# Kernel tuning notes

Hardware: AMD Instinct MI355X
Metric: run time of the kernel (lower is better)

Reference implementation:

```python
import jax, jax.numpy as jnp
import numpy as np

BN_EPS = 1e-5


def setup_inputs() -> dict:
    key = jax.random.key(0)
    ks = jax.random.split(key, 8)
    B, C, H, W = 2, 512, 64, 64
    Ck, Cv = 256, 256
    x = jax.random.normal(ks[0], (B, C, H, W), jnp.float32)
    # f_key/f_query shared 1x1 conv (kaiming, relu)
    wk = jax.random.normal(ks[1], (Ck, C), jnp.float32) * (2.0 / C) ** 0.5
    bk = jnp.zeros((Ck,), jnp.float32)
    bn_gamma = jax.random.uniform(ks[2], (Ck,), jnp.float32, 0.5, 1.5)
    bn_beta = jax.random.normal(ks[3], (Ck,), jnp.float32) * 0.1
    bn_mean = jax.random.normal(ks[4], (Ck,), jnp.float32) * 0.1
    bn_var = jax.random.uniform(ks[5], (Ck,), jnp.float32, 0.5, 1.5)
    # f_value: 3x3 conv then 1x1 conv
    wv1 = jax.random.normal(ks[6], (Cv, C, 3, 3), jnp.float32) * (2.0 / (C * 9)) ** 0.5
    bv1 = jnp.zeros((Cv,), jnp.float32)
    wv2 = jax.random.normal(ks[7], (Cv, Cv), jnp.float32) * (2.0 / Cv) ** 0.5
    bv2 = jnp.zeros((Cv,), jnp.float32)
    return dict(x=x, wk=wk, bk=bk, bn_gamma=bn_gamma, bn_beta=bn_beta,
                bn_mean=bn_mean, bn_var=bn_var, wv1=wv1, bv1=bv1, wv2=wv2, bv2=bv2)


def reference(x, wk, bk, bn_gamma, bn_beta, bn_mean, bn_var, wv1, bv1, wv2, bv2):
    B, C, H, W = x.shape
    Ck, Cv = wk.shape[0], wv1.shape[0]
    N = H * W
    # f_key == f_query: 1x1 conv + BN (inference form) + ReLU
    feat = jnp.einsum('oc,bchw->bohw', wk, x) + bk[:, None, None]
    scale_bn = (bn_gamma / jnp.sqrt(bn_var + BN_EPS))
    feat = (feat - bn_mean[:, None, None]) * scale_bn[:, None, None] + bn_beta[:, None, None]
    feat = jax.nn.relu(feat).reshape(B, Ck, N)  # [B, Ck, N]
    # sim_map = softmax(Ck^-0.5 * Q^T K); Q and K are the same tensor
    sim_map = jax.nn.softmax(jnp.einsum('bcn,bcm->bnm', feat, feat) * (Ck ** -0.5), axis=-1)
    # f_value: conv3x3 + relu + conv1x1 + relu
    v = jax.lax.conv_general_dilated(x, wv1, (1, 1), 'SAME',
                                     dimension_numbers=('NCHW', 'OIHW', 'NCHW'))
    v = jax.nn.relu(v + bv1[:, None, None])
    v = jax.nn.relu(jnp.einsum('oc,bchw->bohw', wv2, v) + bv2[:, None, None])
    v = v.reshape(B, Cv, N)  # [B, Cv, N]
    context = jnp.einsum('bnm,bcm->bcn', sim_map, v).reshape(B, Cv, H, W)
    return context, sim_map
```

## Files before the change

### kernel.cpp

```cpp
#include <hip/hip_runtime.h>
#include <hip/hip_bf16.h>
#include <stdint.h>

typedef unsigned short u16_t;
typedef __attribute__((ext_vector_type(8))) short short8;
typedef __attribute__((ext_vector_type(4))) float f32x4;
typedef __attribute__((ext_vector_type(4))) unsigned short us4;

__device__ __forceinline__ float bf2f(u16_t u) {
  union { unsigned int i; float f; } c; c.i = ((unsigned int)u) << 16; return c.f;
}
__device__ __forceinline__ u16_t f2bf(float f) {
  union { float f; unsigned int i; } c; c.f = f;
  unsigned int x = c.i;
  unsigned int r = x + 0x7fffu + ((x >> 16) & 1u);
  return (u16_t)(r >> 16);
}

__device__ __forceinline__ void gload_lds16(const u16_t* g, u16_t* l) {
  __builtin_amdgcn_global_load_lds(
      (const __attribute__((address_space(1))) void*)g,
      (__attribute__((address_space(3))) void*)(unsigned int)(uintptr_t)l,
      16, 0, 0);
}

struct Seg {
  const u16_t* Ah;
  const u16_t* Al;
  const u16_t* Bh;
  const u16_t* Bl;
  int boff;
};

struct GemmArgs {
  Seg segs[9];
  int nseg;
  int segs_per_split;
  int K;
  int ldA, ldB;
  long long sA, sB;
  float alpha;
  float* outf;
  long long sOut;
  long long sSplit;
  int ldT;
};

template<int BM, int BN, int MODE, bool PADB, bool SYMM, int NCH = 4>
__global__ __launch_bounds__(256, 4) void gemm_tn(GemmArgs args) {
  constexpr int FM = BM / 32, FN = BN / 32;
  constexpr int AH_E = NCH * BM * 8;
  constexpr int AL_E = (MODE == 0) ? NCH * BM * 8 : 8;
  constexpr int BH_E = NCH * BN * 8;
  constexpr int BL_E = (MODE <= 1) ? NCH * BN * 8 : 8;
  constexpr int SM_E = AH_E + AL_E + BH_E + BL_E;
  static_assert(!SYMM || (size_t)SM_E * 2 >= 32 * 132 * 4, "tbuf alias too small");
  __shared__ __align__(16) u16_t smem[SM_E];
  u16_t* aflat_h = smem;
  u16_t* aflat_l = smem + AH_E;
  u16_t* bflat_h = smem + AH_E + AL_E;
  u16_t* bflat_l = smem + AH_E + AL_E + BH_E;

  const int tid = threadIdx.x;
  const int wave = tid >> 6, lane = tid & 63;
  const int lhi = lane >> 4, llo = lane & 15;
  const int wr = wave >> 1, wc = wave & 1;
  int nt, mt, b, split;
  if (SYMM) {
    b = blockIdx.z; split = 0;
    int t = blockIdx.x, r = 0;
    while (t >= 32 - r) { t -= 32 - r; ++r; }
    mt = r; nt = r + t;
  } else {
    nt = blockIdx.x; mt = blockIdx.y;
    b = blockIdx.z & 1; split = blockIdx.z >> 1;
  }
  const int row0 = mt * BM, col0 = nt * BN;

  f32x4 acc[FM][FN];
  const f32x4 zero4 = {0.f, 0.f, 0.f, 0.f};
#pragma unroll
  for (int i = 0; i < FM; ++i)
#pragma unroll
    for (int j = 0; j < FN; ++j) acc[i][j] = zero4;

  constexpr int RA = BM * NCH / 256;
  constexpr int RB = BN * NCH / 256;

  const int s0 = split * args.segs_per_split;
  int s1 = s0 + args.segs_per_split;
  if (s1 > args.nseg) s1 = args.nseg;

  for (int s = s0; s < s1; ++s) {
    const u16_t* Abh = args.segs[s].Ah + (size_t)b * args.sA;
    const u16_t* Abl = args.segs[s].Al + (size_t)b * args.sA;
    const u16_t* Bbh = args.segs[s].Bh + (size_t)b * args.sB;
    const u16_t* Bbl = args.segs[s].Bl + (size_t)b * args.sB;
    const int boff = args.segs[s].boff;
    for (int k0 = 0; k0 < args.K; k0 += NCH * 8) {
      __syncthreads();
#pragma unroll
      for (int r = 0; r < RA; ++r) {
        int idx = r * 256 + tid;
        int chunk = idx / BM, m = idx % BM;
        size_t goff = (size_t)(row0 + m) * args.ldA + (k0 + chunk * 8);
        gload_lds16(Abh + goff, aflat_h + (size_t)idx * 8);
        if (MODE == 0)
          gload_lds16(Abl + goff, aflat_l + (size_t)idx * 8);
      }
#pragma unroll
      for (int r = 0; r < RB; ++r) {
        int idx = r * 256 + tid;
        int chunk = idx / BN, n = idx % BN;
        long long rowi;
        if (PADB) {
          int gn = col0 + n;
          rowi = (long long)((gn >> 6) + 1) * 66 + (gn & 63) + 1 + boff;
        } else {
          rowi = col0 + n;
        }
        size_t goff = (size_t)rowi * args.ldB + (k0 + chunk * 8);
        gload_lds16(Bbh + goff, bflat_h + (size_t)idx * 8);
        if (MODE <= 1)
          gload_lds16(Bbl + goff, bflat_l + (size_t)idx * 8);
      }
      __syncthreads();
#pragma unroll
      for (int kk = 0; kk < NCH / 4; ++kk) {
        const int ckA = (kk * 4 + lhi) * BM;
        const int ckB = (kk * 4 + lhi) * BN;
        short8 afh[FM], afl[FM], bfh[FN], bfl[FN];
#pragma unroll
        for (int i = 0; i < FM; ++i) {
          afh[i] = *(const short8*)(aflat_h + ((size_t)ckA + wr * (BM / 2) + i * 16 + llo) * 8);
          if (MODE == 0)
            afl[i] = *(const short8*)(aflat_l + ((size_t)ckA + wr * (BM / 2) + i * 16 + llo) * 8);
        }
#pragma unroll
        for (int j = 0; j < FN; ++j) {
          bfh[j] = *(const short8*)(bflat_h + ((size_t)ckB + wc * (BN / 2) + j * 16 + llo) * 8);
          if (MODE <= 1)
            bfl[j] = *(const short8*)(bflat_l + ((size_t)ckB + wc * (BN / 2) + j * 16 + llo) * 8);
        }
#pragma unroll
        for (int i = 0; i < FM; ++i)
#pragma unroll
          for (int j = 0; j < FN; ++j) {
            f32x4 t = acc[i][j];
            if (MODE <= 1)
              t = __builtin_amdgcn_mfma_f32_16x16x32_bf16(afh[i], bfl[j], t, 0, 0, 0);
            if (MODE == 0)
              t = __builtin_amdgcn_mfma_f32_16x16x32_bf16(afl[i], bfh[j], t, 0, 0, 0);
            t = __builtin_amdgcn_mfma_f32_16x16x32_bf16(afh[i], bfh[j], t, 0, 0, 0);
            acc[i][j] = t;
          }
      }
    }
  }

  float* outp = args.outf + (size_t)split * args.sSplit + (size_t)b * args.sOut;
#pragma unroll
  for (int i = 0; i < FM; ++i) {
    int mb = row0 + wr * (BM / 2) + i * 16 + lhi * 4;
#pragma unroll
    for (int j = 0; j < FN; ++j) {
      int n = col0 + wc * (BN / 2) + j * 16 + llo;
      f32x4 vv = acc[i][j] * args.alpha;
      *(f32x4*)(outp + (size_t)n * args.ldT + mb) = vv;
    }
  }
  if (SYMM) {
    if (nt != mt) {
      float* tb = (float*)smem;
#pragma unroll
      for (int i = 0; i < FM; ++i) {
        __syncthreads();
#pragma unroll
        for (int j = 0; j < FN; ++j) {
#pragma unroll
          for (int r2 = 0; r2 < 4; ++r2) {
            int trow = wr * 16 + lhi * 4 + r2;
            int tcol = wc * 64 + j * 16 + llo;
            tb[trow * 132 + tcol] = acc[i][j][r2] * args.alpha;
          }
        }
        __syncthreads();
#pragma unroll
        for (int it = 0; it < 4; ++it) {
          int idx = it * 256 + tid;
          int row = idx >> 5, c4 = idx & 31;
          int mg = row0 + (row >> 4) * 64 + i * 16 + (row & 15);
          f32x4 v4 = *(f32x4*)&tb[row * 132 + c4 * 4];
          *(f32x4*)(outp + (size_t)mg * args.ldT + col0 + c4 * 4) = v4;
        }
      }
    }
  }
}

struct Conv3Args {
  const u16_t* W;
  const u16_t* X;
  float* outf;
  long long sOut;
  long long sSplit;
};
__global__ __launch_bounds__(256, 4) void conv3_gemm(Conv3Args a) {
  __shared__ __align__(16) u16_t lA[3][4][128][8];
  __shared__ __align__(16) u16_t lB[4 * 144 * 8];
  const int tid = threadIdx.x;
  const int wave = tid >> 6, lane = tid & 63;
  const int lhi = lane >> 4, llo = lane & 15;
  const int wr = wave >> 1, wc = wave & 1;
  const int nt = blockIdx.x, mt = blockIdx.y;
  const int b = blockIdx.z & 1, ty = blockIdx.z >> 1;
  const int row0 = mt * 128;
  const int base = (2 * nt + ty) * 66;
  const u16_t* Xb = a.X + (size_t)b * 4356 * 512;
  const u16_t* Wt = a.W + (size_t)(ty * 3) * 131072;

  f32x4 acc[4][4];
  const f32x4 zero4 = {0.f, 0.f, 0.f, 0.f};
#pragma unroll
  for (int i = 0; i < 4; ++i)
#pragma unroll
    for (int j = 0; j < 4; ++j) acc[i][j] = zero4;

  for (int k0 = 0; k0 < 512; k0 += 32) {
    __syncthreads();
#pragma unroll
    for (int t = 0; t < 3; ++t)
#pragma unroll
      for (int r = 0; r < 2; ++r) {
        int slot = r * 256 + tid;
        int chunk = slot >> 7, m = slot & 127;
        const u16_t* src = Wt + (size_t)t * 131072 + (size_t)(row0 + m) * 512 + k0 + chunk * 8;
        gload_lds16(src, &lA[t][0][0][0] + (size_t)slot * 8);
      }
#pragma unroll
    for (int r = 0; r < 2; ++r) {
      int idx = r * 256 + tid;
      int chunk = idx / 144, rr = idx % 144;
      gload_lds16(Xb + (size_t)(base + rr) * 512 + k0 + chunk * 8, lB + (size_t)idx * 8);
    }
    if (tid < 64) {
      int idx = 512 + tid;
      int chunk = idx / 144, rr = idx % 144;
      gload_lds16(Xb + (size_t)(base + rr) * 512 + k0 + chunk * 8, lB + (size_t)idx * 8);
    }
    __syncthreads();
#pragma unroll
    for (int t = 0; t < 3; ++t) {
      short8 af[4], bf[4];
#pragma unroll
      for (int i = 0; i < 4; ++i)
        af[i] = *(const short8*)&lA[t][lhi][wr * 64 + i * 16 + llo][0];
#pragma unroll
      for (int j = 0; j < 4; ++j) {
        int rB = wc * 66 + j * 16 + llo + t;
        bf[j] = *(const short8*)(lB + ((size_t)lhi * 144 + rB) * 8);
      }
#pragma unroll
      for (int i = 0; i < 4; ++i)
#pragma unroll
        for (int j = 0; j < 4; ++j)
          acc[i][j] = __builtin_amdgcn_mfma_f32_16x16x32_bf16(af[i], bf[j], acc[i][j], 0, 0, 0);
    }
  }

  float* outp = a.outf + (size_t)ty * a.sSplit + (size_t)b * a.sOut;
#pragma unroll
  for (int i = 0; i < 4; ++i) {
    int mb = row0 + wr * 64 + i * 16 + lhi * 4;
#pragma unroll
    for (int j = 0; j < 4; ++j) {
      int n = (nt << 7) + wc * 64 + j * 16 + llo;
      *(f32x4*)(outp + (size_t)n * 256 + mb) = acc[i][j];
    }
  }
}

template<int LDT, bool PER_COL>
__global__ __launch_bounds__(256) void reduce_split(
    const float* __restrict__ part, long long sSplit, int ns,
    const float* __restrict__ scale, const float* __restrict__ bias,
    u16_t* __restrict__ oh, u16_t* __restrict__ ol, long long total) {
  long long i = ((long long)blockIdx.x * 256 + threadIdx.x) * 4;
  if (i >= total) return;
  f32x4 s = *(const f32x4*)(part + i);
  for (int p = 1; p < ns; ++p) s += *(const f32x4*)(part + (size_t)p * sSplit + i);
  f32x4 v;
  if (PER_COL) {
    int c = (int)(i & (LDT - 1));
    f32x4 bi = *(const f32x4*)(bias + c);
    if (scale) { f32x4 sc = *(const f32x4*)(scale + c); v = s * sc + bi; }
    else v = s + bi;
  } else {
    int r = (int)((i / LDT) & 255);
    float bi = bias[r];
    v = s + bi;
  }
  us4 h, l;
#pragma unroll
  for (int c2 = 0; c2 < 4; ++c2) {
    float vv = v[c2] > 0.f ? v[c2] : 0.f;
    u16_t hh = f2bf(vv);
    h[c2] = hh;
    l[c2] = f2bf(vv - bf2f(hh));
  }
  *(us4*)(oh + i) = h;
  if (ol) *(us4*)(ol + i) = l;
}

__global__ __launch_bounds__(256) void reduce_split_f32(
    const float* __restrict__ part, long long sSplit, int ns,
    float* __restrict__ out, long long total) {
  long long i = ((long long)blockIdx.x * 256 + threadIdx.x) * 4;
  if (i >= total) return;
  f32x4 s = *(const f32x4*)(part + i);
  for (int p = 1; p < ns; ++p) s += *(const f32x4*)(part + (size_t)p * sSplit + i);
  *(f32x4*)(out + i) = s;
}

__global__ __launch_bounds__(256) void softmax_k(float* S, u16_t* P) {
  const int row = blockIdx.x;
  float* Sr = S + (size_t)row * 4096;
  u16_t* Pr = P + (size_t)row * 4096;
  const int t = threadIdx.x;
  const int wave = t >> 6;
  f32x4 v[4];
  float vmax = -3.4e38f;
#pragma unroll
  for (int i = 0; i < 4; ++i) {
    v[i] = ((const f32x4*)Sr)[t + i * 256];
#pragma unroll
    for (int c = 0; c < 4; ++c) vmax = fmaxf(vmax, v[i][c]);
  }
#pragma unroll
  for (int off = 32; off; off >>= 1) vmax = fmaxf(vmax, __shfl_xor(vmax, off));
  __shared__ float red[4];
  if ((t & 63) == 0) red[wave] = vmax;
  __syncthreads();
  vmax = fmaxf(fmaxf(red[0], red[1]), fmaxf(red[2], red[3]));
  float sum = 0.f;
#pragma unroll
  for (int i = 0; i < 4; ++i)
#pragma unroll
    for (int c = 0; c < 4; ++c) { v[i][c] = __expf(v[i][c] - vmax); sum += v[i][c]; }
#pragma unroll
  for (int off = 32; off; off >>= 1) sum += __shfl_xor(sum, off);
  __shared__ float red2[4];
  if ((t & 63) == 0) red2[wave] = sum;
  __syncthreads();
  sum = red2[0] + red2[1] + red2[2] + red2[3];
  float rs = 1.0f / sum;
#pragma unroll
  for (int i = 0; i < 4; ++i) {
    f32x4 o = v[i] * rs;
    ((f32x4*)Sr)[t + i * 256] = o;
    us4 pb;
#pragma unroll
    for (int c = 0; c < 4; ++c) pb[c] = f2bf(o[c]);
    ((us4*)Pr)[t + i * 256] = pb;
  }
}

__global__ __launch_bounds__(256) void xprep(const float* __restrict__ x,
                                             u16_t* __restrict__ xh, u16_t* __restrict__ xl) {
  __shared__ float tile[64][65];
  const int b = blockIdx.z, c0 = blockIdx.y * 64, n0 = blockIdx.x * 64;
  const float* xb = x + ((size_t)b * 512 + c0) * 4096 + n0;
  const int t = threadIdx.x;
  const int tr = t >> 6, tc = t & 63;
#pragma unroll
  for (int rr = 0; rr < 16; ++rr) {
    int ci = tr + rr * 4;
    tile[ci][tc] = xb[(size_t)ci * 4096 + tc];
  }
  __syncthreads();
#pragma unroll
  for (int rr = 0; rr < 16; ++rr) {
    int nj = rr * 4 + tr;
    float v = tile[tc][nj];
    size_t rp = (size_t)(blockIdx.x + 1) * 66 + nj + 1;
    size_t o = ((size_t)b * 4356 + rp) * 512 + c0 + tc;
    u16_t hh = f2bf(v);
    xh[o] = hh;
    xl[o] = f2bf(v - bf2f(hh));
  }
}

__global__ __launch_bounds__(256) void prep_all(
    const float* __restrict__ wk, const float* __restrict__ wv2, const float* __restrict__ wv1,
    const float* __restrict__ g, const float* __restrict__ be, const float* __restrict__ mu,
    const float* __restrict__ var, const float* __restrict__ bkb,
    u16_t* __restrict__ wkh, u16_t* __restrict__ wkl,
    u16_t* __restrict__ w2h, u16_t* __restrict__ w2l,
    u16_t* __restrict__ w1h, float* __restrict__ bnA, float* __restrict__ bnB,
    u16_t* __restrict__ xh, u16_t* __restrict__ xl) {
  long long i = (long long)blockIdx.x * 256 + threadIdx.x;
  if (i < 256) {
    float s = g[i] * rsqrtf(var[i] + 1e-5f);
    bnA[i] = s;
    bnB[i] = (bkb[i] - mu[i]) * s + be[i];
    return;
  }
  i -= 256;
  if (i < 131072) {
    float v = wk[i];
    u16_t hh = f2bf(v);
    wkh[i] = hh; wkl[i] = f2bf(v - bf2f(hh));
    return;
  }
  i -= 131072;
  if (i < 65536) {
    float v = wv2[i];
    u16_t hh = f2bf(v);
    w2h[i] = hh; w2l[i] = f2bf(v - bf2f(hh));
    return;
  }
  i -= 65536;
  if (i < 1179648) {
    int tp = (int)(i / (256 * 512));
    int rem = (int)(i % (256 * 512));
    int o = rem / 512, c = rem % 512;
    w1h[i] = f2bf(wv1[((size_t)o * 512 + c) * 9 + tp]);
    return;
  }
  i -= 1179648;
  if (i < 133120) {
    int blk = (int)(i >> 8), t = (int)(i & 255);
    int rowi = blk % 260, b = blk / 260;
    int rp;
    if (rowi < 66) rp = rowi;
    else if (rowi < 132) rp = 4290 + (rowi - 66);
    else { int g2 = (rowi - 132) >> 1; rp = (g2 + 1) * 66 + ((rowi - 132) & 1) * 65; }
    size_t base = ((size_t)b * 4356 + rp) * 512;
    const us4 z = {0, 0, 0, 0};
    if (t < 128) *(us4*)(xh + base + (size_t)t * 4) = z;
    else *(us4*)(xl + base + (size_t)(t - 128) * 4) = z;
  }
}

extern "C" void kernel_launch(void* const* d_in, const int* in_sizes, int n_in,
                              void* d_out, int out_size, void* d_ws, size_t ws_size,
                              hipStream_t stream) {
  (void)in_sizes; (void)n_in; (void)out_size; (void)ws_size;
  const float* x   = (const float*)d_in[0];
  const float* wk  = (const float*)d_in[1];
  const float* bk  = (const float*)d_in[2];
  const float* gam = (const float*)d_in[3];
  const float* bet = (const float*)d_in[4];
  const float* mu  = (const float*)d_in[5];
  const float* var = (const float*)d_in[6];
  const float* wv1 = (const float*)d_in[7];
  const float* bv1 = (const float*)d_in[8];
  const float* wv2 = (const float*)d_in[9];
  const float* bv2 = (const float*)d_in[10];

  const int B = 2;
  const size_t XT_E  = (size_t)B * 4356 * 512;
  const size_t WK_E  = 256 * 512;
  const size_t WV1_E = 9ull * 256 * 512;
  const size_t WV2_E = 256 * 256;
  const size_t FT_E  = (size_t)B * 4096 * 256;
  const size_t P_E   = (size_t)B * 4096 * 4096;

  size_t off = 0;
  auto carve = [&](size_t bytes) -> char* {
    off = (off + 255) & ~(size_t)255;
    char* p = (char*)d_ws + off;
    off += bytes;
    return p;
  };
  u16_t* xh  = (u16_t*)carve(XT_E * 2);
  u16_t* xl  = (u16_t*)carve(XT_E * 2);
  u16_t* wkh = (u16_t*)carve(WK_E * 2);
  u16_t* wkl = (u16_t*)carve(WK_E * 2);
  u16_t* w1h = (u16_t*)carve(WV1_E * 2);
  u16_t* w2h = (u16_t*)carve(WV2_E * 2);
  u16_t* w2l = (u16_t*)carve(WV2_E * 2);
  u16_t* fth = (u16_t*)carve(FT_E * 2);
  u16_t* ftl = (u16_t*)carve(FT_E * 2);
  u16_t* v1h = (u16_t*)carve(FT_E * 2);
  u16_t* v1l = (u16_t*)carve(FT_E * 2);
  u16_t* vh  = (u16_t*)carve(FT_E * 2);
  u16_t* Pb  = (u16_t*)carve(P_E * 2);
  float* bnA = (float*)carve(256 * 4);
  float* bnB = (float*)carve(256 * 4);

  float* big_part = (float*)Pb;
  float* pv_part  = (float*)d_ws;

  float* ctx = (float*)d_out;
  float* sim = (float*)d_out + (size_t)B * 256 * 4096;

  const long long FT_LL = (long long)FT_E;

  prep_all<<<5897, 256, 0, stream>>>(wk, wv2, wv1, gam, bet, mu, var, bk,
                                     wkh, wkl, w2h, w2l, w1h, bnA, bnB, xh, xl);
  xprep<<<dim3(64, 8, 2), 256, 0, stream>>>(x, xh, xl);

  {
    GemmArgs a = {};
    a.segs[0] = {wkh,       wkl,       xh,       xl,       0};
    a.segs[1] = {wkh + 256, wkl + 256, xh + 256, xl + 256, 0};
    a.nseg = 2; a.segs_per_split = 1; a.K = 256; a.ldA = 512; a.ldB = 512;
    a.sA = 0; a.sB = (long long)4356 * 512; a.alpha = 1.f;
    a.outf = big_part; a.sOut = (long long)4096 * 256; a.sSplit = FT_LL; a.ldT = 256;
    gemm_tn<64, 128, 0, true, false><<<dim3(32, 4, 4), 256, 0, stream>>>(a);
    reduce_split<256, true><<<2048, 256, 0, stream>>>(big_part, FT_LL, 2, bnA, bnB, fth, ftl, FT_LL);
  }
  {
    GemmArgs a = {};
    a.segs[0] = {fth, nullptr, fth, ftl, 0};
    a.nseg = 1; a.segs_per_split = 1; a.K = 256; a.ldA = 256; a.ldB = 256;
    a.sA = (long long)4096 * 256; a.sB = (long long)4096 * 256; a.alpha = 0.0625f;
    a.outf = sim; a.sOut = (long long)4096 * 4096; a.sSplit = 0; a.ldT = 4096;
    gemm_tn<128, 128, 1, false, true><<<dim3(528, 1, 2), 256, 0, stream>>>(a);
  }
  {
    Conv3Args a;
    a.W = w1h; a.X = xh;
    a.outf = big_part; a.sOut = (long long)4096 * 256; a.sSplit = FT_LL;
    conv3_gemm<<<dim3(32, 2, 6), 256, 0, stream>>>(a);
    reduce_split<256, true><<<2048, 256, 0, stream>>>(big_part, FT_LL, 3, nullptr, bv1, v1h, v1l, FT_LL);
  }
  {
    GemmArgs a = {};
    a.segs[0] = {v1h,       v1l,       w2h,       w2l,       0};
    a.segs[1] = {v1h + 128, v1l + 128, w2h + 128, w2l + 128, 0};
    a.nseg = 2; a.segs_per_split = 1; a.K = 128; a.ldA = 256; a.ldB = 256;
    a.sA = (long long)4096 * 256; a.sB = 0; a.alpha = 1.f;
    a.outf = big_part; a.sOut = (long long)256 * 4096; a.sSplit = FT_LL; a.ldT = 4096;
    gemm_tn<128, 64, 0, false, false><<<dim3(4, 32, 4), 256, 0, stream>>>(a);
    reduce_split<4096, false><<<2048, 256, 0, stream>>>(big_part, FT_LL, 2, nullptr, bv2, vh, nullptr, FT_LL);
  }
  softmax_k<<<B * 4096, 256, 0, stream>>>(sim, Pb);
  {
    GemmArgs a = {};
    for (int q = 0; q < 4; ++q)
      a.segs[q] = {Pb + (size_t)q * 1024, nullptr, vh + (size_t)q * 1024, nullptr, 0};
    a.nseg = 4; a.segs_per_split = 1; a.K = 1024; a.ldA = 4096; a.ldB = 4096;
    a.sA = (long long)4096 * 4096; a.sB = (long long)256 * 4096; a.alpha = 1.f;
    a.outf = pv_part; a.sOut = (long long)256 * 4096; a.sSplit = FT_LL; a.ldT = 4096;
    gemm_tn<128, 128, 2, false, false, 8><<<dim3(2, 32, 8), 256, 0, stream>>>(a);
    reduce_split_f32<<<2048, 256, 0, stream>>>(pv_part, FT_LL, 4, ctx, FT_LL);
  }
}
```

Before: 265.9 us.

## Fuse softmax into symmetric QK GEMM via recompute with partial row stats

After: 295.4 us. 11.1% more time.

```diff
diff --git a/kernel.cpp b/kernel.cpp
--- a/kernel.cpp
+++ b/kernel.cpp
@@ -46,7 +46,7 @@
   int ldT;
 };
 
-template<int BM, int BN, int MODE, bool PADB, bool SYMM, int NCH = 4>
+template<int BM, int BN, int MODE, bool PADB, int NCH = 4>
 __global__ __launch_bounds__(256, 4) void gemm_tn(GemmArgs args) {
   constexpr int FM = BM / 32, FN = BN / 32;
   constexpr int AH_E = NCH * BM * 8;
@@ -54,7 +54,6 @@
   constexpr int BH_E = NCH * BN * 8;
   constexpr int BL_E = (MODE <= 1) ? NCH * BN * 8 : 8;
   constexpr int SM_E = AH_E + AL_E + BH_E + BL_E;
-  static_assert(!SYMM || (size_t)SM_E * 2 >= 32 * 132 * 4, "tbuf alias too small");
   __shared__ __align__(16) u16_t smem[SM_E];
   u16_t* aflat_h = smem;
   u16_t* aflat_l = smem + AH_E;
@@ -65,16 +64,8 @@
   const int wave = tid >> 6, lane = tid & 63;
   const int lhi = lane >> 4, llo = lane & 15;
   const int wr = wave >> 1, wc = wave & 1;
-  int nt, mt, b, split;
-  if (SYMM) {
-    b = blockIdx.z; split = 0;
-    int t = blockIdx.x, r = 0;
-    while (t >= 32 - r) { t -= 32 - r; ++r; }
-    mt = r; nt = r + t;
-  } else {
-    nt = blockIdx.x; mt = blockIdx.y;
-    b = blockIdx.z & 1; split = blockIdx.z >> 1;
-  }
+  const int nt = blockIdx.x, mt = blockIdx.y;
+  const int b = blockIdx.z & 1, split = blockIdx.z >> 1;
   const int row0 = mt * BM, col0 = nt * BN;
 
   f32x4 acc[FM][FN];
@@ -169,19 +160,191 @@
       *(f32x4*)(outp + (size_t)n * args.ldT + mb) = vv;
     }
   }
-  if (SYMM) {
-    if (nt != mt) {
+}
+
+struct QkArgs {
+  const u16_t* fh;
+  const u16_t* fl;
+  float* pmax;
+  float* psum;
+  const float* mx;
+  const float* rs;
+  float* sim;
+  u16_t* Pb;
+};
+
+template<int EPI>
+__global__ __launch_bounds__(256, 4) void qk_symm(QkArgs args) {
+  __shared__ __align__(16) u16_t smem[3 * 4096];
+  u16_t* aflat_h = smem;
+  u16_t* bflat_h = smem + 4096;
+  u16_t* bflat_l = smem + 8192;
+
+  const int tid = threadIdx.x;
+  const int wave = tid >> 6, lane = tid & 63;
+  const int lhi = lane >> 4, llo = lane & 15;
+  const int wr = wave >> 1, wc = wave & 1;
+  const int b = blockIdx.z;
+  int t = blockIdx.x, r = 0;
+  while (t >= 32 - r) { t -= 32 - r; ++r; }
+  const int mt = r, nt = r + t;
+  const int row0 = mt * 128, col0 = nt * 128;
+
+  const u16_t* Fh = args.fh + (size_t)b * 4096 * 256;
+  const u16_t* Fl = args.fl + (size_t)b * 4096 * 256;
+
+  f32x4 acc[4][4];
+  const f32x4 zero4 = {0.f, 0.f, 0.f, 0.f};
+#pragma unroll
+  for (int i = 0; i < 4; ++i)
+#pragma unroll
+    for (int j = 0; j < 4; ++j) acc[i][j] = zero4;
+
+  for (int k0 = 0; k0 < 256; k0 += 32) {
+    __syncthreads();
+#pragma unroll
+    for (int rr = 0; rr < 2; ++rr) {
+      int idx = rr * 256 + tid;
+      int chunk = idx >> 7, m = idx & 127;
+      gload_lds16(Fh + (size_t)(row0 + m) * 256 + k0 + chunk * 8, aflat_h + (size_t)idx * 8);
+      gload_lds16(Fh + (size_t)(col0 + m) * 256 + k0 + chunk * 8, bflat_h + (size_t)idx * 8);
+      gload_lds16(Fl + (size_t)(col0 + m) * 256 + k0 + chunk * 8, bflat_l + (size_t)idx * 8);
+    }
+    __syncthreads();
+    short8 afh[4], bfh[4], bfl[4];
+#pragma unroll
+    for (int i = 0; i < 4; ++i)
+      afh[i] = *(const short8*)(aflat_h + ((size_t)lhi * 128 + wr * 64 + i * 16 + llo) * 8);
+#pragma unroll
+    for (int j = 0; j < 4; ++j) {
+      bfh[j] = *(const short8*)(bflat_h + ((size_t)lhi * 128 + wc * 64 + j * 16 + llo) * 8);
+      bfl[j] = *(const short8*)(bflat_l + ((size_t)lhi * 128 + wc * 64 + j * 16 + llo) * 8);
+    }
+#pragma unroll
+    for (int i = 0; i < 4; ++i)
+#pragma unroll
+      for (int j = 0; j < 4; ++j) {
+        f32x4 tt = acc[i][j];
+        tt = __builtin_amdgcn_mfma_f32_16x16x32_bf16(afh[i], bfl[j], tt, 0, 0, 0);
+        tt = __builtin_amdgcn_mfma_f32_16x16x32_bf16(afh[i], bfh[j], tt, 0, 0, 0);
+        acc[i][j] = tt;
+      }
+  }
+#pragma unroll
+  for (int i = 0; i < 4; ++i)
+#pragma unroll
+    for (int j = 0; j < 4; ++j) acc[i][j] *= 0.0625f;
+
+  if (EPI == 0) {
+    __syncthreads();
+    float* nmax_l = (float*)smem;
+    float* nsum_l = nmax_l + 256;
+    float* mmax_l = nsum_l + 256;
+    float* msum_l = mmax_l + 256;
+#pragma unroll
+    for (int j = 0; j < 4; ++j) {
+      float m_ = -3.4e38f;
+#pragma unroll
+      for (int i = 0; i < 4; ++i)
+#pragma unroll
+        for (int r2 = 0; r2 < 4; ++r2) m_ = fmaxf(m_, acc[i][j][r2]);
+      m_ = fmaxf(m_, __shfl_xor(m_, 16));
+      m_ = fmaxf(m_, __shfl_xor(m_, 32));
+      float su = 0.f;
+#pragma unroll
+      for (int i = 0; i < 4; ++i)
+#pragma unroll
+        for (int r2 = 0; r2 < 4; ++r2) su += __expf(acc[i][j][r2] - m_);
+      su += __shfl_xor(su, 16);
+      su += __shfl_xor(su, 32);
+      if (lhi == 0) {
+        int nl = wc * 64 + j * 16 + llo;
+        nmax_l[wr * 128 + nl] = m_;
+        nsum_l[wr * 128 + nl] = su;
+      }
+    }
+    if (mt != nt) {
+#pragma unroll
+      for (int i = 0; i < 4; ++i)
+#pragma unroll
+        for (int r2 = 0; r2 < 4; ++r2) {
+          float m_ = fmaxf(fmaxf(acc[0][0][r2], 0.f) * 0.f - 3.4e38f, -3.4e38f);
+          m_ = -3.4e38f;
+#pragma unroll
+          for (int j = 0; j < 4; ++j) m_ = fmaxf(m_, acc[i][j][r2]);
+          m_ = fmaxf(m_, __shfl_xor(m_, 1));
+          m_ = fmaxf(m_, __shfl_xor(m_, 2));
+          m_ = fmaxf(m_, __shfl_xor(m_, 4));
+          m_ = fmaxf(m_, __shfl_xor(m_, 8));
+          float su = 0.f;
+#pragma unroll
+          for (int j = 0; j < 4; ++j) su += __expf(acc[i][j][r2] - m_);
+          su += __shfl_xor(su, 1);
+          su += __shfl_xor(su, 2);
+          su += __shfl_xor(su, 4);
+          su += __shfl_xor(su, 8);
+          if (llo == 0) {
+            int ml = wr * 64 + i * 16 + lhi * 4 + r2;
+            mmax_l[wc * 128 + ml] = m_;
+            msum_l[wc * 128 + ml] = su;
+          }
+        }
+    }
+    __syncthreads();
+    if (tid < 128) {
+      float a0 = nmax_l[tid], a1 = nmax_l[128 + tid];
+      float g = fmaxf(a0, a1);
+      float su = nsum_l[tid] * __expf(a0 - g) + nsum_l[128 + tid] * __expf(a1 - g);
+      size_t o = (size_t)mt * 8192 + (size_t)b * 4096 + col0 + tid;
+      args.pmax[o] = g;
+      args.psum[o] = su;
+    } else if (mt != nt) {
+      int ml = tid - 128;
+      float a0 = mmax_l[ml], a1 = mmax_l[128 + ml];
+      float g = fmaxf(a0, a1);
+      float su = msum_l[ml] * __expf(a0 - g) + msum_l[128 + ml] * __expf(a1 - g);
+      size_t o = (size_t)nt * 8192 + (size_t)b * 4096 + row0 + ml;
+      args.pmax[o] = g;
+      args.psum[o] = su;
+    }
+  } else {
+    const float* MX = args.mx + (size_t)b * 4096;
+    const float* RS = args.rs + (size_t)b * 4096;
+    float* simb = args.sim + (size_t)b * 4096 * 4096;
+    u16_t* Pbb = args.Pb + (size_t)b * 4096 * 4096;
+#pragma unroll
+    for (int i = 0; i < 4; ++i) {
+      int mb = row0 + wr * 64 + i * 16 + lhi * 4;
+#pragma unroll
+      for (int j = 0; j < 4; ++j) {
+        int n = col0 + wc * 64 + j * 16 + llo;
+        float mxn = MX[n], rsn = RS[n];
+        f32x4 o;
+        us4 h;
+#pragma unroll
+        for (int r2 = 0; r2 < 4; ++r2) {
+          float e = __expf(acc[i][j][r2] - mxn) * rsn;
+          o[r2] = e;
+          h[r2] = f2bf(e);
+        }
+        *(f32x4*)(simb + (size_t)n * 4096 + mb) = o;
+        *(us4*)(Pbb + (size_t)n * 4096 + mb) = h;
+      }
+    }
+    if (mt != nt) {
       float* tb = (float*)smem;
 #pragma unroll
-      for (int i = 0; i < FM; ++i) {
+      for (int i = 0; i < 4; ++i) {
         __syncthreads();
 #pragma unroll
-        for (int j = 0; j < FN; ++j) {
-#pragma unroll
-          for (int r2 = 0; r2 < 4; ++r2) {
-            int trow = wr * 16 + lhi * 4 + r2;
+        for (int r2 = 0; r2 < 4; ++r2) {
+          int m = row0 + wr * 64 + i * 16 + lhi * 4 + r2;
+          float mxm = MX[m], rsm = RS[m];
+          int trow = wr * 16 + lhi * 4 + r2;
+#pragma unroll
+          for (int j = 0; j < 4; ++j) {
             int tcol = wc * 64 + j * 16 + llo;
-            tb[trow * 132 + tcol] = acc[i][j][r2] * args.alpha;
+            tb[trow * 132 + tcol] = __expf(acc[i][j][r2] - mxm) * rsm;
           }
         }
         __syncthreads();
@@ -191,11 +354,30 @@
           int row = idx >> 5, c4 = idx & 31;
           int mg = row0 + (row >> 4) * 64 + i * 16 + (row & 15);
           f32x4 v4 = *(f32x4*)&tb[row * 132 + c4 * 4];
-          *(f32x4*)(outp + (size_t)mg * args.ldT + col0 + c4 * 4) = v4;
+          *(f32x4*)(simb + (size_t)mg * 4096 + col0 + c4 * 4) = v4;
+          us4 h;
+#pragma unroll
+          for (int c = 0; c < 4; ++c) h[c] = f2bf(v4[c]);
+          *(us4*)(Pbb + (size_t)mg * 4096 + col0 + c4 * 4) = h;
         }
       }
     }
   }
+}
+
+__global__ __launch_bounds__(256) void stat_reduce(
+    const float* __restrict__ pmax, const float* __restrict__ psum,
+    float* __restrict__ mx, float* __restrict__ rs) {
+  int row = blockIdx.x * 256 + threadIdx.x;
+  float g = -3.4e38f;
+#pragma unroll
+  for (int c = 0; c < 32; ++c) g = fmaxf(g, pmax[(size_t)c * 8192 + row]);
+  float su = 0.f;
+#pragma unroll
+  for (int c = 0; c < 32; ++c)
+    su += psum[(size_t)c * 8192 + row] * __expf(pmax[(size_t)c * 8192 + row] - g);
+  mx[row] = g;
+  rs[row] = 1.0f / su;
 }
 
 struct Conv3Args {
@@ -322,49 +504,6 @@
   *(f32x4*)(out + i) = s;
 }
 
-__global__ __launch_bounds__(256) void softmax_k(float* S, u16_t* P) {
-  const int row = blockIdx.x;
-  float* Sr = S + (size_t)row * 4096;
-  u16_t* Pr = P + (size_t)row * 4096;
-  const int t = threadIdx.x;
-  const int wave = t >> 6;
-  f32x4 v[4];
-  float vmax = -3.4e38f;
-#pragma unroll
-  for (int i = 0; i < 4; ++i) {
-    v[i] = ((const f32x4*)Sr)[t + i * 256];
-#pragma unroll
-    for (int c = 0; c < 4; ++c) vmax = fmaxf(vmax, v[i][c]);
-  }
-#pragma unroll
-  for (int off = 32; off; off >>= 1) vmax = fmaxf(vmax, __shfl_xor(vmax, off));
-  __shared__ float red[4];
-  if ((t & 63) == 0) red[wave] = vmax;
-  __syncthreads();
-  vmax = fmaxf(fmaxf(red[0], red[1]), fmaxf(red[2], red[3]));
-  float sum = 0.f;
-#pragma unroll
-  for (int i = 0; i < 4; ++i)
-#pragma unroll
-    for (int c = 0; c < 4; ++c) { v[i][c] = __expf(v[i][c] - vmax); sum += v[i][c]; }
-#pragma unroll
-  for (int off = 32; off; off >>= 1) sum += __shfl_xor(sum, off);
-  __shared__ float red2[4];
-  if ((t & 63) == 0) red2[wave] = sum;
-  __syncthreads();
-  sum = red2[0] + red2[1] + red2[2] + red2[3];
-  float rs = 1.0f / sum;
-#pragma unroll
-  for (int i = 0; i < 4; ++i) {
-    f32x4 o = v[i] * rs;
-    ((f32x4*)Sr)[t + i * 256] = o;
-    us4 pb;
-#pragma unroll
-    for (int c = 0; c < 4; ++c) pb[c] = f2bf(o[c]);
-    ((us4*)Pr)[t + i * 256] = pb;
-  }
-}
-
 __global__ __launch_bounds__(256) void xprep(const float* __restrict__ x,
                                              u16_t* __restrict__ xh, u16_t* __restrict__ xl) {
   __shared__ float tile[64][65];
@@ -486,6 +625,10 @@
   u16_t* v1l = (u16_t*)carve(FT_E * 2);
   u16_t* vh  = (u16_t*)carve(FT_E * 2);
   u16_t* Pb  = (u16_t*)carve(P_E * 2);
+  float* pmax = (float*)carve(32 * 8192 * 4);
+  float* psum = (float*)carve(32 * 8192 * 4);
+  float* mxb  = (float*)carve(8192 * 4);
+  float* rsb  = (float*)carve(8192 * 4);
   float* bnA = (float*)carve(256 * 4);
   float* bnB = (float*)carve(256 * 4);
 
@@ -508,16 +651,8 @@
     a.nseg = 2; a.segs_per_split = 1; a.K = 256; a.ldA = 512; a.ldB = 512;
     a.sA = 0; a.sB = (long long)4356 * 512; a.alpha = 1.f;
     a.outf = big_part; a.sOut = (long long)4096 * 256; a.sSplit = FT_LL; a.ldT = 256;
-    gemm_tn<64, 128, 0, true, false><<<dim3(32, 4, 4), 256, 0, stream>>>(a);
+    gemm_tn<64, 128, 0, true><<<dim3(32, 4, 4), 256, 0, stream>>>(a);
     reduce_split<256, true><<<2048, 256, 0, stream>>>(big_part, FT_LL, 2, bnA, bnB, fth, ftl, FT_LL);
-  }
-  {
-    GemmArgs a = {};
-    a.segs[0] = {fth, nullptr, fth, ftl, 0};
-    a.nseg = 1; a.segs_per_split = 1; a.K = 256; a.ldA = 256; a.ldB = 256;
-    a.sA = (long long)4096 * 256; a.sB = (long long)4096 * 256; a.alpha = 0.0625f;
-    a.outf = sim; a.sOut = (long long)4096 * 4096; a.sSplit = 0; a.ldT = 4096;
-    gemm_tn<128, 128, 1, false, true><<<dim3(528, 1, 2), 256, 0, stream>>>(a);
   }
   {
     Conv3Args a;
@@ -533,10 +668,17 @@
     a.nseg = 2; a.segs_per_split = 1; a.K = 128; a.ldA = 256; a.ldB = 256;
     a.sA = (long long)4096 * 256; a.sB = 0; a.alpha = 1.f;
     a.outf = big_part; a.sOut = (long long)256 * 4096; a.sSplit = FT_LL; a.ldT = 4096;
-    gemm_tn<128, 64, 0, false, false><<<dim3(4, 32, 4), 256, 0, stream>>>(a);
+    gemm_tn<128, 64, 0, false><<<dim3(4, 32, 4), 256, 0, stream>>>(a);
     reduce_split<4096, false><<<2048, 256, 0, stream>>>(big_part, FT_LL, 2, nullptr, bv2, vh, nullptr, FT_LL);
   }
-  softmax_k<<<B * 4096, 256, 0, stream>>>(sim, Pb);
+  {
+    QkArgs a = {};
+    a.fh = fth; a.fl = ftl; a.pmax = pmax; a.psum = psum;
+    a.mx = mxb; a.rs = rsb; a.sim = sim; a.Pb = Pb;
+    qk_symm<0><<<dim3(528, 1, 2), 256, 0, stream>>>(a);
+    stat_reduce<<<32, 256, 0, stream>>>(pmax, psum, mxb, rsb);
+    qk_symm<1><<<dim3(528, 1, 2), 256, 0, stream>>>(a);
+  }
   {
     GemmArgs a = {};
     for (int q = 0; q < 4; ++q)
@@ -544,7 +686,7 @@
     a.nseg = 4; a.segs_per_split = 1; a.K = 1024; a.ldA = 4096; a.ldB = 4096;
     a.sA = (long long)4096 * 4096; a.sB = (long long)256 * 4096; a.alpha = 1.f;
     a.outf = pv_part; a.sOut = (long long)256 * 4096; a.sSplit = FT_LL; a.ldT = 4096;
-    gemm_tn<128, 128, 2, false, false, 8><<<dim3(2, 32, 8), 256, 0, stream>>>(a);
+    gemm_tn<128, 128, 2, false, 8><<<dim3(2, 32, 8), 256, 0, stream>>>(a);
     reduce_split_f32<<<2048, 256, 0, stream>>>(pv_part, FT_LL, 4, ctx, FT_LL);
   }
 }
```
